# Optimization experiments

Measured on AMD Instinct MI355X. Metric: run time of the kernel, lower is better.

## Reference

```python
import jax, jax.numpy as jnp
import numpy as np

B, L, D = 2, 2048, 768
H = 12
HD = D // H  # 64
SCALE = HD ** -0.5


def setup_inputs() -> dict:
    key = jax.random.key(0)
    k1, k2, k3 = jax.random.split(key, 3)
    x = jax.random.normal(k1, (B, L, D), dtype=jnp.float32)
    mask = jnp.ones((B, L), dtype=jnp.int32)
    # nn.Linear weights: [out_features, in_features]
    Wqkv = jax.random.normal(k2, (3 * D, D), dtype=jnp.float32) * (D ** -0.5)
    bqkv = jnp.zeros((3 * D,), dtype=jnp.float32)
    Wout = jax.random.normal(k3, (D, D), dtype=jnp.float32) * (D ** -0.5)
    bout = jnp.zeros((D,), dtype=jnp.float32)
    return {"x": x, "mask": mask, "Wqkv": Wqkv, "bqkv": bqkv, "Wout": Wout, "bout": bout}


def reference(x, mask, Wqkv, bqkv, Wout, bout):
    Bx, Lx, Dx = x.shape
    # qkv projection: [B,L,3D] -> [3,B,H,L,HD]
    qkv = x @ Wqkv.T + bqkv
    qkv = qkv.reshape(Bx, Lx, 3, H, HD).transpose(2, 0, 3, 1, 4)
    q, k, v = qkv[0], qkv[1], qkv[2]
    # scores [B,H,L,L]
    attn = jnp.einsum('bhqd,bhkd->bhqk', q, k) * SCALE
    attn = jnp.where(mask[:, None, None, :] == 0, -jnp.inf, attn)
    attn = jax.nn.softmax(attn, axis=-1)
    # dropout p=0.0 -> identity
    out = jnp.einsum('bhqk,bhkd->bhqd', attn, v)
    out = out.transpose(0, 2, 1, 3).reshape(Bx, Lx, Dx)
    return out @ Wout.T + bout
```

## Files before the change

### kernel.cpp

```cpp
#include <hip/hip_runtime.h>
#include <hip/hip_bf16.h>

#define DEV __device__ __forceinline__

typedef __bf16 bf16_t;
typedef bf16_t bf16x8 __attribute__((ext_vector_type(8)));
typedef float f32x4 __attribute__((ext_vector_type(4)));
typedef float f32x16 __attribute__((ext_vector_type(16)));
typedef unsigned int u32x4 __attribute__((ext_vector_type(4)));

constexpr int Bc = 2, Lc = 2048, Dc = 768, Hc = 12, HDc = 64;
constexpr int NTOK = Bc * Lc;
constexpr int QKVN = 3 * Dc;
constexpr float ATT_SCALE = 0.125f;
constexpr float LOG2E = 1.44269504088896f;

DEV unsigned short f2bf(float f) {
  unsigned int u = __builtin_bit_cast(unsigned int, f);
  u += 0x7FFFu + ((u >> 16) & 1u);
  return (unsigned short)(u >> 16);
}

DEV bf16x8 ld16(const unsigned short* p) {
  return __builtin_bit_cast(bf16x8, *reinterpret_cast<const u32x4*>(p));
}

DEV unsigned cvtpk(float lo, float hi) {
  unsigned r;
  asm("v_cvt_pk_bf16_f32 %0, %1, %2" : "=v"(r) : "v"(lo), "v"(hi));
  return r;
}

DEV void gload16(const unsigned short* g, unsigned short* l) {
  __builtin_amdgcn_global_load_lds(
      (const __attribute__((address_space(1))) unsigned int*)g,
      (__attribute__((address_space(3))) unsigned int*)l, 16, 0, 0);
}

__global__ __launch_bounds__(256) void prep_kernel(
    const float* __restrict__ x, const float* __restrict__ Wqkv,
    const float* __restrict__ Wout, const int* __restrict__ mask,
    unsigned short* __restrict__ xb, unsigned short* __restrict__ wqkvb,
    unsigned short* __restrict__ woutb, float* __restrict__ mb,
    int* __restrict__ mflag) {
  const int bid = blockIdx.x, tid = threadIdx.x;
  const float* src; unsigned short* dst; int base;
  if (bid < 3072)      { src = x;    dst = xb;    base = bid; }
  else if (bid < 4800) { src = Wqkv; dst = wqkvb; base = bid - 3072; }
  else if (bid < 5376) { src = Wout; dst = woutb; base = bid - 4800; }
  else {
    int i = (bid - 5376) * 256 + tid;
    int mv = mask[i];
    mb[i] = mv ? 0.f : -1e30f;
    unsigned long long anyz = __ballot(mv == 0);
    if ((tid & 63) == 0) mflag[i >> 6] = (anyz != 0ull) ? 1 : 0;
    return;
  }
  int i = (base * 256 + tid) * 4;
  float4 v = *reinterpret_cast<const float4*>(src + i);
  ushort4 o;
  o.x = f2bf(v.x); o.y = f2bf(v.y); o.z = f2bf(v.z); o.w = f2bf(v.w);
  *reinterpret_cast<ushort4*>(dst + i) = o;
}

template <int MODE>
__global__ __launch_bounds__(256) void gemm_bt(
    const unsigned short* __restrict__ A,
    const unsigned short* __restrict__ Bw,
    const float* __restrict__ bias,
    unsigned short* __restrict__ qb, unsigned short* __restrict__ kb,
    unsigned short* __restrict__ vtb,
    float* __restrict__ Y,
    int M, int N, int K) {
  constexpr int BM = 128, BN = 128, BK = 64;
  __shared__ alignas(16) unsigned short a_lds[BM * BK];
  __shared__ alignas(16) unsigned short b_lds[BN * BK];
  __shared__ alignas(16) unsigned short qk_patch[(MODE == 0) ? 4 : 1][16][72];

  const int tid = threadIdx.x;
  const int lane = tid & 63;
  const int l15 = lane & 15, lg = lane >> 4;
  const int wave = tid >> 6;
  const int wr = wave >> 1, wc = wave & 1;

  const int ntiles = N / BN;
  const int m0 = (blockIdx.x / ntiles) * BM;
  const int n0 = (blockIdx.x % ntiles) * BN;

  f32x4 acc[4][4] = {};

  for (int k0 = 0; k0 < K; k0 += BK) {
#pragma unroll
    for (int i = 0; i < 4; ++i) {
      int cc = i * 256 + tid;
      int row = cc >> 3, col = (cc & 7) * 8;
      gload16(A + (size_t)(m0 + row) * K + k0 + col, &a_lds[(i * 256 + wave * 64) * 8]);
      gload16(Bw + (size_t)(n0 + row) * K + k0 + col, &b_lds[(i * 256 + wave * 64) * 8]);
    }
    __syncthreads();
#pragma unroll
    for (int kk = 0; kk < 2; ++kk) {
      bf16x8 af[4], bfr[4];
#pragma unroll
      for (int m = 0; m < 4; ++m) {
        int row = wr * 64 + m * 16 + l15;
        af[m] = ld16(&a_lds[row * BK + kk * 32 + lg * 8]);
      }
#pragma unroll
      for (int n = 0; n < 4; ++n) {
        int row = wc * 64 + n * 16 + l15;
        bfr[n] = ld16(&b_lds[row * BK + kk * 32 + lg * 8]);
      }
#pragma unroll
      for (int m = 0; m < 4; ++m)
#pragma unroll
        for (int n = 0; n < 4; ++n)
          acc[m][n] = __builtin_amdgcn_mfma_f32_16x16x32_bf16(af[m], bfr[n], acc[m][n], 0, 0, 0);
    }
    __syncthreads();
  }

  if constexpr (MODE == 0) {
    const int base_col = n0 + wc * 64;
    const int s = base_col / Dc;
    const int h = (base_col % Dc) >> 6;
    if (s == 2) {
#pragma unroll
      for (int m = 0; m < 4; ++m) {
        int lq = m0 + wr * 64 + m * 16 + lg * 4;
        int b = lq >> 11, lql = lq & 2047;
#pragma unroll
        for (int n = 0; n < 4; ++n) {
          int d = n * 16 + l15;
          float bv = bias[base_col + n * 16 + l15];
          ushort4 o;
#pragma unroll
          for (int j = 0; j < 4; ++j)
            ((unsigned short*)&o)[j] = f2bf(acc[m][n][j] + bv);
          *reinterpret_cast<ushort4*>(
              vtb + ((size_t)(b * Hc + h) * HDc + d) * Lc + lql) = o;
        }
      }
    } else {
      unsigned short* dst = (s == 0) ? qb : kb;
      const float sc = (s == 0) ? (ATT_SCALE * LOG2E) : 1.0f;
#pragma unroll
      for (int m = 0; m < 4; ++m) {
#pragma unroll
        for (int n = 0; n < 4; ++n) {
          float bv = bias[base_col + n * 16 + l15];
#pragma unroll
          for (int j = 0; j < 4; ++j)
            qk_patch[wave][lg * 4 + j][n * 16 + l15] =
                f2bf((acc[m][n][j] + bv) * sc);
        }
#pragma unroll
        for (int i = 0; i < 2; ++i) {
          int task = i * 64 + lane;
          int r = task >> 3, ch = task & 7;
          int lq = m0 + wr * 64 + m * 16 + r;
          int b = lq >> 11, lql = lq & 2047;
          u32x4 v = *reinterpret_cast<const u32x4*>(&qk_patch[wave][r][ch * 8]);
          *reinterpret_cast<u32x4*>(
              dst + ((size_t)(b * Hc + h) * Lc + lql) * HDc + ch * 8) = v;
        }
      }
    }
  } else {
#pragma unroll
    for (int m = 0; m < 4; ++m) {
      int row_base = m0 + wr * 64 + m * 16 + lg * 4;
#pragma unroll
      for (int n = 0; n < 4; ++n) {
        int col = n0 + wc * 64 + n * 16 + l15;
        float bv = bias[col];
#pragma unroll
        for (int j = 0; j < 4; ++j)
          Y[(size_t)(row_base + j) * Dc + col] = acc[m][n][j] + bv;
      }
    }
  }
}

__global__ __launch_bounds__(256) void attn_kernel(
    const unsigned short* __restrict__ qb,
    const unsigned short* __restrict__ kb,
    const unsigned short* __restrict__ vtb,
    const float* __restrict__ mb,
    const int* __restrict__ mflag,
    unsigned short* __restrict__ aout) {
  __shared__ alignas(16) unsigned short k_lds[3][4096];
  __shared__ alignas(16) unsigned short v_lds[3][4096];
  __shared__ float l_lds[2][32];
  const int tid = threadIdx.x;
  const int lane = tid & 63;
  const int l31 = lane & 31;
  const int hi = lane >> 5;
  const int wave = tid >> 6;
  const int ws = wave & 1;
  const int g = wave >> 1;
  const int f = blockIdx.x;
  const int loc = f >> 3;
  const int bh = (f & 7) * 3 + (loc >> 5);
  const int b = bh / Hc, h = bh % Hc;
  const int q0 = (loc & 31) * 64 + ws * 32;

  const unsigned short* Kbh = kb + (size_t)bh * Lc * HDc;
  const unsigned short* Vbh = vtb + (size_t)bh * HDc * Lc;
  const float* mbb = mb + b * Lc + hi * 4;
  const int* mfp = mflag + b * (Lc / 64);

  unsigned long long mbits;
  {
    int mv = (lane < 32) ? mfp[lane] : 0;
    mbits = __ballot(mv != 0);
  }

  bf16x8 qf[4];
  {
    const unsigned short* Qp = qb + ((size_t)bh * Lc + q0 + l31) * HDc + hi * 8;
#pragma unroll
    for (int c = 0; c < 4; ++c) qf[c] = ld16(Qp + c * 16);
  }

  f32x16 accO[2] = {};
  float l_run = 0.f;

  const int j0 = wave * 2, j1 = j0 + 1;
  const int r80 = j0 * 8 + (lane >> 3), r81 = r80 + 8;
  const int csw0 = (((lane & 7) ^ (lane >> 3) ^ (j0 & 3))) << 3;
  const int csw1 = (((lane & 7) ^ (lane >> 3) ^ (j1 & 3))) << 3;
  const unsigned short* kp0 = Kbh + (size_t)r80 * HDc + csw0;
  const unsigned short* kp1 = Kbh + (size_t)r81 * HDc + csw1;
  const unsigned short* vp0 = Vbh + (size_t)r80 * Lc + csw0;
  const unsigned short* vp1 = Vbh + (size_t)r81 * Lc + csw1;

#define STAGE(buf)                                \
  {                                               \
    gload16(kp0, &k_lds[buf][j0 * 512]);          \
    gload16(kp1, &k_lds[buf][j1 * 512]);          \
    gload16(vp0, &v_lds[buf][j0 * 512]);          \
    gload16(vp1, &v_lds[buf][j1 * 512]);          \
    kp0 += 64 * HDc; kp1 += 64 * HDc;             \
    vp0 += 64; vp1 += 64;                         \
  }

  STAGE(0)
  STAGE(1)

  const int swz = ((l31 & 7) ^ (l31 >> 3)) << 3;

  constexpr int NSTEP = Lc / 64;
  int cs = 0;
  for (int t = 0; t < NSTEP; ++t) {
    if (t < NSTEP - 1) {
      asm volatile("s_waitcnt vmcnt(4)" ::: "memory");
    } else {
      asm volatile("s_waitcnt vmcnt(0)" ::: "memory");
    }
    __builtin_amdgcn_s_barrier();
    __builtin_amdgcn_sched_barrier(0);
    int ss = cs + 2; if (ss >= 3) ss -= 3;
    if (t + 2 < NSTEP) STAGE(ss)

    const unsigned short* kl = &k_lds[cs][0];
    const unsigned short* vl = &v_lds[cs][0];

    f32x16 s = {};
    __builtin_amdgcn_s_setprio(1);
#pragma unroll
    for (int c = 0; c < 4; ++c) {
      int ch = (((c * 2 + hi) << 3) ^ swz);
      s = __builtin_amdgcn_mfma_f32_32x32x16_bf16(
          ld16(kl + (g * 32 + l31) * 64 + ch), qf[c], s, 0, 0, 0);
    }
    __builtin_amdgcn_s_setprio(0);
    if ((mbits >> t) & 1ull) {
      const int kvt = t * 64 + g * 32;
#pragma unroll
      for (int gg = 0; gg < 4; ++gg) {
        float4 m0v = *reinterpret_cast<const float4*>(mbb + kvt + gg * 8);
        s[gg * 4 + 0] += m0v.x; s[gg * 4 + 1] += m0v.y;
        s[gg * 4 + 2] += m0v.z; s[gg * 4 + 3] += m0v.w;
      }
    }
    float rs0 = 0.f, rs1 = 0.f, rs2 = 0.f, rs3 = 0.f;
#pragma unroll
    for (int i = 0; i < 16; i += 4) {
      s[i] = __builtin_amdgcn_exp2f(s[i]);         rs0 += s[i];
      s[i + 1] = __builtin_amdgcn_exp2f(s[i + 1]); rs1 += s[i + 1];
      s[i + 2] = __builtin_amdgcn_exp2f(s[i + 2]); rs2 += s[i + 2];
      s[i + 3] = __builtin_amdgcn_exp2f(s[i + 3]); rs3 += s[i + 3];
    }
    float rs = (rs0 + rs1) + (rs2 + rs3);
    rs += __shfl_xor(rs, 32);
    l_run += rs;
    bf16x8 pf[2];
#pragma unroll
    for (int c = 0; c < 2; ++c) {
      const int o = c * 8;
      unsigned pk01 = cvtpk(s[o + 0], s[o + 1]);
      unsigned pk23 = cvtpk(s[o + 2], s[o + 3]);
      unsigned pk45 = cvtpk(s[o + 4], s[o + 5]);
      unsigned pk67 = cvtpk(s[o + 6], s[o + 7]);
      asm("v_permlane32_swap_b32 %0, %1" : "+v"(pk01), "+v"(pk45));
      asm("v_permlane32_swap_b32 %0, %1" : "+v"(pk23), "+v"(pk67));
      u32x4 w = {pk01, pk23, pk45, pk67};
      pf[c] = __builtin_bit_cast(bf16x8, w);
    }
    __builtin_amdgcn_s_setprio(1);
#pragma unroll
    for (int dt = 0; dt < 2; ++dt) {
#pragma unroll
      for (int c = 0; c < 2; ++c) {
        int ch = (((g * 4 + c * 2 + hi) << 3) ^ swz);
        accO[dt] = __builtin_amdgcn_mfma_f32_32x32x16_bf16(
            ld16(vl + (dt * 32 + l31) * 64 + ch), pf[c], accO[dt], 0, 0, 0);
      }
    }
    __builtin_amdgcn_s_setprio(0);
    ++cs; if (cs == 3) cs = 0;
  }

  __syncthreads();
  float* mO = (float*)&k_lds[0][0];
  if (g == 1) {
#pragma unroll
    for (int dt = 0; dt < 2; ++dt)
#pragma unroll
      for (int i = 0; i < 16; ++i)
        mO[(ws * 32 + dt * 16 + i) * 64 + lane] = accO[dt][i];
    if (hi == 0) l_lds[ws][l31] = l_run;
  }
  __syncthreads();
  if (g == 0) {
    float rl = 1.0f / (l_run + l_lds[ws][l31]);
    const int q = q0 + l31;
    unsigned short* op = aout + ((size_t)(b * Lc + q)) * Dc + h * HDc;
#pragma unroll
    for (int dt = 0; dt < 2; ++dt)
#pragma unroll
      for (int gg = 0; gg < 4; ++gg) {
        ushort4 o;
#pragma unroll
        for (int j = 0; j < 4; ++j) {
          int i = gg * 4 + j;
          float v = (accO[dt][i] + mO[(ws * 32 + dt * 16 + i) * 64 + lane]) * rl;
          ((unsigned short*)&o)[j] = f2bf(v);
        }
        *reinterpret_cast<ushort4*>(op + dt * 32 + gg * 8 + hi * 4) = o;
      }
  }
}

extern "C" void kernel_launch(void* const* d_in, const int* in_sizes, int n_in,
                              void* d_out, int out_size, void* d_ws, size_t ws_size,
                              hipStream_t stream) {
  const float* x    = (const float*)d_in[0];
  const int*   mask = (const int*)d_in[1];
  const float* Wqkv = (const float*)d_in[2];
  const float* bqkv = (const float*)d_in[3];
  const float* Wout = (const float*)d_in[4];
  const float* bout = (const float*)d_in[5];
  float* out = (float*)d_out;

  constexpr size_t NX   = (size_t)NTOK * Dc;
  constexpr size_t NWQ  = (size_t)QKVN * Dc;
  constexpr size_t NWO  = (size_t)Dc * Dc;
  unsigned short* w = (unsigned short*)d_ws;
  unsigned short* xb    = w;            w += NX;
  unsigned short* wqkvb = w;            w += NWQ;
  unsigned short* woutb = w;            w += NWO;
  unsigned short* qbuf  = w;            w += NX;
  unsigned short* kbuf  = w;            w += NX;
  unsigned short* vtb   = w;            w += NX;
  unsigned short* aoutb = w;            w += NX;
  float* mbf = (float*)w;               w += 2 * NTOK;
  int* mflag = (int*)w;

  prep_kernel<<<5392, 256, 0, stream>>>(x, Wqkv, Wout, mask, xb, wqkvb, woutb, mbf, mflag);

  gemm_bt<0><<<(NTOK / 128) * (QKVN / 128), 256, 0, stream>>>(
      xb, wqkvb, bqkv, qbuf, kbuf, vtb, nullptr, NTOK, QKVN, Dc);

  attn_kernel<<<dim3(768), 256, 0, stream>>>(qbuf, kbuf, vtb, mbf, mflag, aoutb);

  gemm_bt<1><<<(NTOK / 128) * (Dc / 128), 256, 0, stream>>>(
      aoutb, woutb, bout, nullptr, nullptr, nullptr, out, NTOK, Dc, Dc);
}
```

Measured before the change: 115.0 us.

## Software-pipeline QK^T one step ahead and compute row sums via MFMA

Restructures the attention loop so the QK^T MFMAs for tile t+1 are issued while softmax and PV for tile t run. K gets a 4-deep LDS ring and V a 2-deep ring with separate staging macros, and the wait/barrier moves to the end of each iteration. Row sums are no longer built from VALU adds plus a cross-lane shuffle; they come from two extra MFMAs that multiply a ones matrix by the probability fragments. The intent is to overlap matrix and exponent work and take reductions off the VALU. The cost is more registers for the second score tile and accumulator, four extra MFMAs per step, and a tighter vmcnt accounting that is easy to get wrong.

```diff
diff --git a/kernel.cpp b/kernel.cpp
--- a/kernel.cpp
+++ b/kernel.cpp
@@ -189,8 +189,8 @@
     const float* __restrict__ mb,
     const int* __restrict__ mflag,
     unsigned short* __restrict__ aout) {
-  __shared__ alignas(16) unsigned short k_lds[3][4096];
-  __shared__ alignas(16) unsigned short v_lds[3][4096];
+  __shared__ alignas(16) unsigned short k_lds[4][4096];
+  __shared__ alignas(16) unsigned short v_lds[2][4096];
   __shared__ float l_lds[2][32];
   const int tid = threadIdx.x;
   const int lane = tid & 63;
@@ -223,8 +223,14 @@
     for (int c = 0; c < 4; ++c) qf[c] = ld16(Qp + c * 16);
   }
 
+  bf16x8 onesf;
+  {
+    u32x4 ow = {0x3F803F80u, 0x3F803F80u, 0x3F803F80u, 0x3F803F80u};
+    onesf = __builtin_bit_cast(bf16x8, ow);
+  }
+
   f32x16 accO[2] = {};
-  float l_run = 0.f;
+  f32x16 accL = {};
 
   const int j0 = wave * 2, j1 = j0 + 1;
   const int r80 = j0 * 8 + (lane >> 3), r81 = r80 + 8;
@@ -235,46 +241,51 @@
   const unsigned short* vp0 = Vbh + (size_t)r80 * Lc + csw0;
   const unsigned short* vp1 = Vbh + (size_t)r81 * Lc + csw1;
 
-#define STAGE(buf)                                \
+#define STAGEK(buf)                               \
   {                                               \
     gload16(kp0, &k_lds[buf][j0 * 512]);          \
     gload16(kp1, &k_lds[buf][j1 * 512]);          \
+    kp0 += 64 * HDc; kp1 += 64 * HDc;             \
+  }
+#define STAGEV(buf)                               \
+  {                                               \
     gload16(vp0, &v_lds[buf][j0 * 512]);          \
     gload16(vp1, &v_lds[buf][j1 * 512]);          \
-    kp0 += 64 * HDc; kp1 += 64 * HDc;             \
     vp0 += 64; vp1 += 64;                         \
   }
 
-  STAGE(0)
-  STAGE(1)
-
   const int swz = ((l31 & 7) ^ (l31 >> 3)) << 3;
+  const int krow = (g * 32 + l31) * 64;
+
+  STAGEK(0) STAGEK(1) STAGEV(0)
+  asm volatile("s_waitcnt vmcnt(0)" ::: "memory");
+  __builtin_amdgcn_s_barrier();
+  f32x16 s = {};
+#pragma unroll
+  for (int c = 0; c < 4; ++c) {
+    int ch = (((c * 2 + hi) << 3) ^ swz);
+    s = __builtin_amdgcn_mfma_f32_32x32x16_bf16(
+        ld16(&k_lds[0][0] + krow + ch), qf[c], s, 0, 0, 0);
+  }
+  STAGEK(2) STAGEV(1)
 
   constexpr int NSTEP = Lc / 64;
-  int cs = 0;
   for (int t = 0; t < NSTEP; ++t) {
-    if (t < NSTEP - 1) {
-      asm volatile("s_waitcnt vmcnt(4)" ::: "memory");
-    } else {
-      asm volatile("s_waitcnt vmcnt(0)" ::: "memory");
-    }
-    __builtin_amdgcn_s_barrier();
-    __builtin_amdgcn_sched_barrier(0);
-    int ss = cs + 2; if (ss >= 3) ss -= 3;
-    if (t + 2 < NSTEP) STAGE(ss)
-
-    const unsigned short* kl = &k_lds[cs][0];
-    const unsigned short* vl = &v_lds[cs][0];
-
-    f32x16 s = {};
-    __builtin_amdgcn_s_setprio(1);
-#pragma unroll
-    for (int c = 0; c < 4; ++c) {
-      int ch = (((c * 2 + hi) << 3) ^ swz);
-      s = __builtin_amdgcn_mfma_f32_32x32x16_bf16(
-          ld16(kl + (g * 32 + l31) * 64 + ch), qf[c], s, 0, 0, 0);
-    }
-    __builtin_amdgcn_s_setprio(0);
+    if (t + 3 < NSTEP) STAGEK((t + 3) & 3)
+
+    f32x16 s2 = {};
+    if (t + 1 < NSTEP) {
+      const unsigned short* kl = &k_lds[(t + 1) & 3][0];
+      __builtin_amdgcn_s_setprio(1);
+#pragma unroll
+      for (int c = 0; c < 4; ++c) {
+        int ch = (((c * 2 + hi) << 3) ^ swz);
+        s2 = __builtin_amdgcn_mfma_f32_32x32x16_bf16(
+            ld16(kl + krow + ch), qf[c], s2, 0, 0, 0);
+      }
+      __builtin_amdgcn_s_setprio(0);
+    }
+
     if ((mbits >> t) & 1ull) {
       const int kvt = t * 64 + g * 32;
 #pragma unroll
@@ -284,17 +295,8 @@
         s[gg * 4 + 2] += m0v.z; s[gg * 4 + 3] += m0v.w;
       }
     }
-    float rs0 = 0.f, rs1 = 0.f, rs2 = 0.f, rs3 = 0.f;
-#pragma unroll
-    for (int i = 0; i < 16; i += 4) {
-      s[i] = __builtin_amdgcn_exp2f(s[i]);         rs0 += s[i];
-      s[i + 1] = __builtin_amdgcn_exp2f(s[i + 1]); rs1 += s[i + 1];
-      s[i + 2] = __builtin_amdgcn_exp2f(s[i + 2]); rs2 += s[i + 2];
-      s[i + 3] = __builtin_amdgcn_exp2f(s[i + 3]); rs3 += s[i + 3];
-    }
-    float rs = (rs0 + rs1) + (rs2 + rs3);
-    rs += __shfl_xor(rs, 32);
-    l_run += rs;
+#pragma unroll
+    for (int i = 0; i < 16; ++i) s[i] = __builtin_amdgcn_exp2f(s[i]);
     bf16x8 pf[2];
 #pragma unroll
     for (int c = 0; c < 2; ++c) {
@@ -308,21 +310,35 @@
       u32x4 w = {pk01, pk23, pk45, pk67};
       pf[c] = __builtin_bit_cast(bf16x8, w);
     }
-    __builtin_amdgcn_s_setprio(1);
-#pragma unroll
-    for (int dt = 0; dt < 2; ++dt) {
-#pragma unroll
-      for (int c = 0; c < 2; ++c) {
-        int ch = (((g * 4 + c * 2 + hi) << 3) ^ swz);
-        accO[dt] = __builtin_amdgcn_mfma_f32_32x32x16_bf16(
-            ld16(vl + (dt * 32 + l31) * 64 + ch), pf[c], accO[dt], 0, 0, 0);
-      }
-    }
-    __builtin_amdgcn_s_setprio(0);
-    ++cs; if (cs == 3) cs = 0;
+    accL = __builtin_amdgcn_mfma_f32_32x32x16_bf16(onesf, pf[0], accL, 0, 0, 0);
+    accL = __builtin_amdgcn_mfma_f32_32x32x16_bf16(onesf, pf[1], accL, 0, 0, 0);
+    {
+      const unsigned short* vl = &v_lds[t & 1][0];
+      __builtin_amdgcn_s_setprio(1);
+#pragma unroll
+      for (int dt = 0; dt < 2; ++dt) {
+#pragma unroll
+        for (int c = 0; c < 2; ++c) {
+          int ch = (((g * 4 + c * 2 + hi) << 3) ^ swz);
+          accO[dt] = __builtin_amdgcn_mfma_f32_32x32x16_bf16(
+              ld16(vl + (dt * 32 + l31) * 64 + ch), pf[c], accO[dt], 0, 0, 0);
+        }
+      }
+      __builtin_amdgcn_s_setprio(0);
+    }
+    if (t < NSTEP - 3) {
+      asm volatile("s_waitcnt vmcnt(2)" ::: "memory");
+    } else {
+      asm volatile("s_waitcnt vmcnt(0)" ::: "memory");
+    }
+    __builtin_amdgcn_s_barrier();
+    __builtin_amdgcn_sched_barrier(0);
+    if (t + 2 < NSTEP) STAGEV((t) & 1)
+    s = s2;
   }
 
   __syncthreads();
+  const float l_run = accL[0];
   float* mO = (float*)&k_lds[0][0];
   if (g == 1) {
 #pragma unroll
```

Measured after the change: 113.0 us. About the same (-1.8%).
